# Kernel optimization log

Hardware: AMD Instinct MI355X
Metric: run time of the kernel (lower is better)

The kernel has to match this reference:

```python
import jax, jax.numpy as jnp
import numpy as np

NUM_HEADS = 16
EMB = 1024
HEAD_DIM = EMB // NUM_HEADS


def setup_inputs() -> dict:
    key = jax.random.key(0)
    ks = jax.random.split(key, 9)
    N, L = 2, 2048
    return {
        "keys": jax.random.normal(ks[0], (N, L, EMB), dtype=jnp.float32),
        "queries": jax.random.normal(ks[1], (N, L, EMB), dtype=jnp.float32),
        "values": jax.random.normal(ks[2], (N, L, EMB), dtype=jnp.float32),
        "mask": jax.random.randint(ks[3], (N, L), 0, 2, dtype=jnp.int32),
        "Wk": jax.random.normal(ks[4], (HEAD_DIM, HEAD_DIM), dtype=jnp.float32) * 0.05,
        "Wq": jax.random.normal(ks[5], (HEAD_DIM, HEAD_DIM), dtype=jnp.float32) * 0.05,
        "Wv": jax.random.normal(ks[6], (HEAD_DIM, HEAD_DIM), dtype=jnp.float32) * 0.05,
        "Wo": jax.random.normal(ks[7], (EMB, EMB), dtype=jnp.float32) * 0.02,
        "bo": jax.random.normal(ks[8], (EMB,), dtype=jnp.float32) * 0.02,
    }


def reference(keys, queries, values, mask, Wk, Wq, Wv, Wo, bo):
    N, Q, E = queries.shape
    H, D = NUM_HEADS, HEAD_DIM
    # reshape to heads: [N, L, H, D]
    k = keys.reshape(N, -1, H, D) @ Wk.T
    q = queries.reshape(N, -1, H, D) @ Wq.T
    # faithful to source bug: values are the v-projection of the projected queries
    v = q @ Wv.T
    # energy: [N, H, Q, K]
    energy = jnp.einsum("nqhd,nkhd->nhqk", q, k)
    m = mask[:, None, None, :]  # [N,1,1,K]
    energy = jnp.where(m == 0, jnp.float32(-1e20), energy)
    p = jax.nn.softmax(energy / jnp.sqrt(jnp.float32(E)), axis=3)
    attn = jnp.einsum("nhqk,nkhd->nqhd", p, v).reshape(N, Q, E)
    return attn @ Wo.T + bo
```

## Files before the change

kernel.cpp:

```cpp
#include <hip/hip_runtime.h>
#include <hip/hip_bf16.h>
#include <cmath>

constexpr int N_ = 2;
constexpr int L_ = 2048;
constexpr int H_ = 16;
constexpr int E_ = 1024;
constexpr int ROWS_ = N_ * L_ * H_;
constexpr float KSCALE = 0.04508422002778010648f;

typedef __attribute__((ext_vector_type(8))) short bf16x8;
typedef __attribute__((ext_vector_type(4))) float f32x4;
typedef unsigned short ushort_t;
#define MFMA16(a, b, c) __builtin_amdgcn_mfma_f32_16x16x32_bf16(a, b, c, 0, 0, 0)

__device__ __forceinline__ unsigned short f2bf(float x) {
    union { float f; unsigned u; } v; v.f = x;
    return (unsigned short)((v.u + 0x7fffu + ((v.u >> 16) & 1u)) >> 16);
}
__device__ __forceinline__ unsigned pack2(float a, float b) {
    __hip_bfloat162 t = __float22bfloat162_rn(make_float2(a, b));
    union { __hip_bfloat162 h; unsigned u; } v; v.h = t;
    return v.u;
}
__device__ __forceinline__ void plswap32(unsigned &a, unsigned &b) {
    asm("v_permlane32_swap_b32 %0, %1" : "+v"(a), "+v"(b));
}
__device__ __forceinline__ void plswap16(unsigned &a, unsigned &b) {
    asm("v_permlane16_swap_b32 %0, %1" : "+v"(a), "+v"(b));
}

__global__ __launch_bounds__(256) void proj_kernel(
    const float* __restrict__ keys, const float* __restrict__ queries,
    const float* __restrict__ Wk, const float* __restrict__ Wq, const float* __restrict__ Wv,
    ushort_t* __restrict__ qo, ushort_t* __restrict__ ko, ushort_t* __restrict__ vto)
{
    constexpr int P = 72;
    __shared__ __align__(16) ushort_t Xq[64 * P];
    __shared__ __align__(16) ushort_t Xk[64 * P];
    __shared__ __align__(16) ushort_t Wqs[64 * P];
    __shared__ __align__(16) ushort_t Wks[64 * P];
    __shared__ __align__(16) ushort_t Wvs[64 * P];
    const int tid = threadIdx.x;
    const int lt = blockIdx.x & 31;
    const int h  = (blockIdx.x >> 5) & 15;
    const int n  = blockIdx.x >> 9;
    const int r0 = tid >> 4, c4 = (tid & 15) * 4;

#pragma unroll
    for (int j = 0; j < 4; ++j) {
        const int r = r0 + 16 * j;
        const size_t xoff = (size_t)(n * L_ + lt * 64 + r) * E_ + h * 64 + c4;
        const float4 xq = *(const float4*)&queries[xoff];
        const float4 xk = *(const float4*)&keys[xoff];
        const float4 wq = *(const float4*)&Wq[r * 64 + c4];
        const float4 wk = *(const float4*)&Wk[r * 64 + c4];
        const float4 wv = *(const float4*)&Wv[r * 64 + c4];
        *(uint2*)&Xq[r * P + c4]  = make_uint2(pack2(xq.x, xq.y), pack2(xq.z, xq.w));
        *(uint2*)&Xk[r * P + c4]  = make_uint2(pack2(xk.x, xk.y), pack2(xk.z, xk.w));
        *(uint2*)&Wqs[r * P + c4] = make_uint2(pack2(wq.x, wq.y), pack2(wq.z, wq.w));
        *(uint2*)&Wks[r * P + c4] = make_uint2(pack2(wk.x, wk.y), pack2(wk.z, wk.w));
        *(uint2*)&Wvs[r * P + c4] = make_uint2(pack2(wv.x, wv.y), pack2(wv.z, wv.w));
    }
    __syncthreads();

    const int wave = tid >> 6, lane = tid & 63;
    const int quad = lane >> 4, l16 = lane & 15;
    const int arow = (wave * 16 + l16) * P;
    const f32x4 zero = (f32x4){0.f, 0.f, 0.f, 0.f};

    bf16x8 a0 = *(const bf16x8*)&Xq[arow + quad * 8];
    bf16x8 a1 = *(const bf16x8*)&Xq[arow + 32 + quad * 8];
    bf16x8 c0 = *(const bf16x8*)&Xk[arow + quad * 8];
    bf16x8 c1 = *(const bf16x8*)&Xk[arow + 32 + quad * 8];
    f32x4 qf[4], kf[4];
#pragma unroll
    for (int nt = 0; nt < 4; ++nt) {
        const int brow = (nt * 16 + l16) * P;
        f32x4 acc = MFMA16(a0, *(const bf16x8*)&Wqs[brow + quad * 8], zero);
        qf[nt] = MFMA16(a1, *(const bf16x8*)&Wqs[brow + 32 + quad * 8], acc);
        acc = MFMA16(c0, *(const bf16x8*)&Wks[brow + quad * 8], zero);
        kf[nt] = MFMA16(c1, *(const bf16x8*)&Wks[brow + 32 + quad * 8], acc);
    }
    __syncthreads();

    const int crow = wave * 16 + quad * 4;
#pragma unroll
    for (int nt = 0; nt < 4; ++nt)
#pragma unroll
        for (int reg = 0; reg < 4; ++reg) {
            Xq[(crow + reg) * P + nt * 16 + l16]  = f2bf(qf[nt][reg]);
            Wqs[(crow + reg) * P + nt * 16 + l16] = f2bf(kf[nt][reg] * KSCALE);
        }
    asm volatile("s_waitcnt lgkmcnt(0)" ::: "memory");

    bf16x8 va0 = *(const bf16x8*)&Xq[arow + quad * 8];
    bf16x8 va1 = *(const bf16x8*)&Xq[arow + 32 + quad * 8];
    f32x4 vf[4];
#pragma unroll
    for (int nt = 0; nt < 4; ++nt) {
        const int brow = (nt * 16 + l16) * P;
        f32x4 acc = MFMA16(va0, *(const bf16x8*)&Wvs[brow + quad * 8], zero);
        vf[nt] = MFMA16(va1, *(const bf16x8*)&Wvs[brow + 32 + quad * 8], acc);
    }
#pragma unroll
    for (int nt = 0; nt < 4; ++nt)
#pragma unroll
        for (int reg = 0; reg < 4; ++reg)
            Xk[(nt * 16 + l16) * P + crow + reg] = f2bf(vf[nt][reg]);
    __syncthreads();

#pragma unroll
    for (int j = 0; j < 4; ++j) {
        const int r = r0 + 16 * j;
        const size_t qkoff = (size_t)(n * L_ + lt * 64 + r) * E_ + h * 64 + c4;
        *(uint2*)&qo[qkoff] = *(const uint2*)&Xq[r * P + c4];
        *(uint2*)&ko[qkoff] = *(const uint2*)&Wqs[r * P + c4];
        const size_t vtoff = ((size_t)(n * H_ + h) * 64 + r) * L_ + lt * 64 + c4;
        *(uint2*)&vto[vtoff] = *(const uint2*)&Xk[r * P + c4];
    }
}

__global__ __launch_bounds__(256) void attn_kernel(
    const ushort_t* __restrict__ q, const ushort_t* __restrict__ k,
    const ushort_t* __restrict__ vt, const float* __restrict__ maskf,
    ushort_t* __restrict__ attn)
{
    constexpr int P = 72;
    __shared__ __align__(16) ushort_t Ks[2][64 * P];
    __shared__ __align__(16) ushort_t VTs[2][64 * P];
    __shared__ float Ls[128];

    const int g = blockIdx.x;
    const int xcd = g & 7, j0 = g >> 3;
    const int nh = xcd * 4 + (j0 & 3);
    const int qt = j0 >> 2;
    const int n = nh >> 4, h = nh & 15;

    const int tid = threadIdx.x;
    const int wave = tid >> 6, lane = tid & 63;
    const int l16 = lane & 15, quad = lane >> 4;
    const int r8 = tid >> 3, c8 = (tid & 7) * 8;

    const ushort_t* kh = k  + (size_t)n * L_ * E_ + h * 64;
    const ushort_t* vh = vt + (size_t)(n * H_ + h) * 64 * L_;
    const float*    mh = maskf + n * L_;
    const size_t qrow0 = (size_t)n * L_ + qt * 128 + wave * 32;

    bf16x8 qb[2][2];
#pragma unroll
    for (int s = 0; s < 2; ++s)
#pragma unroll
        for (int c = 0; c < 2; ++c)
            qb[s][c] = *(const bf16x8*)&q[(qrow0 + s * 16 + l16) * E_ + h * 64 + c * 32 + quad * 8];

    uint4 kr[2], vr[2];
#pragma unroll
    for (int j = 0; j < 2; ++j) {
        const int r = r8 + 32 * j;
        kr[j] = *(const uint4*)&kh[(size_t)r * E_ + c8];
        vr[j] = *(const uint4*)&vh[(size_t)r * L_ + c8];
    }
    f32x4 mf[4];
#pragma unroll
    for (int mk = 0; mk < 4; ++mk) mf[mk] = *(const f32x4*)&mh[mk * 16 + quad * 4];

#pragma unroll
    for (int j = 0; j < 2; ++j) {
        const int r = r8 + 32 * j;
        *(uint4*)&Ks[0][r * P + c8]  = kr[j];
        *(uint4*)&VTs[0][r * P + c8] = vr[j];
    }
    __syncthreads();

    float lacc[2] = {0.f, 0.f};
    f32x4 O[2][4];
#pragma unroll
    for (int s = 0; s < 2; ++s)
#pragma unroll
        for (int dt = 0; dt < 4; ++dt) O[s][dt] = (f32x4){0.f, 0.f, 0.f, 0.f};

    for (int t = 0; t < 32; ++t) {
        const int cur = t & 1, nxt = cur ^ 1;
        const int tn = (t < 31) ? t + 1 : 31;

#pragma unroll
        for (int j = 0; j < 2; ++j) {
            const int r = r8 + 32 * j;
            kr[j] = *(const uint4*)&kh[(size_t)(tn * 64 + r) * E_ + c8];
            vr[j] = *(const uint4*)&vh[(size_t)r * L_ + tn * 64 + c8];
        }
        f32x4 mfn[4];
#pragma unroll
        for (int mk = 0; mk < 4; ++mk)
            mfn[mk] = *(const f32x4*)&mh[tn * 64 + mk * 16 + quad * 4];

        bf16x8 kA[4][2];
#pragma unroll
        for (int mk = 0; mk < 4; ++mk)
#pragma unroll
            for (int c = 0; c < 2; ++c)
                kA[mk][c] = *(const bf16x8*)&Ks[cur][(mk * 16 + l16) * P + c * 32 + quad * 8];

        f32x4 sA[2][4];
#pragma unroll
        for (int s = 0; s < 2; ++s)
#pragma unroll
            for (int mk = 0; mk < 4; ++mk) {
                f32x4 acc = mf[mk];
                acc = MFMA16(kA[mk][0], qb[s][0], acc);
                sA[s][mk] = MFMA16(kA[mk][1], qb[s][1], acc);
            }

        bf16x8 vB[4][2];
#pragma unroll
        for (int dt = 0; dt < 4; ++dt)
#pragma unroll
            for (int c = 0; c < 2; ++c)
                vB[dt][c] = *(const bf16x8*)&VTs[cur][(dt * 16 + l16) * P + c * 32 + quad * 8];

        bf16x8 pa[2][2];
#pragma unroll
        for (int s = 0; s < 2; ++s) {
            unsigned u[4][2];
#pragma unroll
            for (int mk = 0; mk < 4; ++mk) {
                const float p0 = __builtin_amdgcn_exp2f(sA[s][mk][0]);
                const float p1 = __builtin_amdgcn_exp2f(sA[s][mk][1]);
                const float p2 = __builtin_amdgcn_exp2f(sA[s][mk][2]);
                const float p3 = __builtin_amdgcn_exp2f(sA[s][mk][3]);
                lacc[s] += (p0 + p1) + (p2 + p3);
                u[mk][0] = pack2(p0, p1);
                u[mk][1] = pack2(p2, p3);
            }
#pragma unroll
            for (int c = 0; c < 2; ++c) {
                union { unsigned w[4]; bf16x8 v; } pw;
#pragma unroll
                for (int hh = 0; hh < 2; ++hh) {
                    unsigned a = u[2 * c][hh], b = u[2 * c + 1][hh];
                    plswap32(a, b);
                    plswap16(a, b);
                    pw.w[hh] = a; pw.w[2 + hh] = b;
                }
                pa[s][c] = pw.v;
            }
        }

#pragma unroll
        for (int s = 0; s < 2; ++s)
#pragma unroll
            for (int dt = 0; dt < 4; ++dt) {
                O[s][dt] = MFMA16(pa[s][0], vB[dt][0], O[s][dt]);
                O[s][dt] = MFMA16(pa[s][1], vB[dt][1], O[s][dt]);
            }

#pragma unroll
        for (int j = 0; j < 2; ++j) {
            const int r = r8 + 32 * j;
            *(uint4*)&Ks[nxt][r * P + c8]  = kr[j];
            *(uint4*)&VTs[nxt][r * P + c8] = vr[j];
        }
#pragma unroll
        for (int mk = 0; mk < 4; ++mk) mf[mk] = mfn[mk];
        __syncthreads();
    }

#pragma unroll
    for (int s = 0; s < 2; ++s) {
        float v = lacc[s];
        v += __shfl_xor(v, 16);
        v += __shfl_xor(v, 32);
        if (quad == 0) Ls[wave * 32 + s * 16 + l16] = 1.f / v;
    }
    asm volatile("s_waitcnt lgkmcnt(0)" ::: "memory");
    f32x4 linv[2];
#pragma unroll
    for (int s = 0; s < 2; ++s) linv[s] = *(const f32x4*)&Ls[wave * 32 + s * 16 + quad * 4];

#pragma unroll
    for (int s = 0; s < 2; ++s)
#pragma unroll
        for (int dt = 0; dt < 4; ++dt)
#pragma unroll
            for (int reg = 0; reg < 4; ++reg) {
                const size_t row = qrow0 + s * 16 + quad * 4 + reg;
                attn[row * E_ + h * 64 + dt * 16 + l16] = f2bf(O[s][dt][reg] * linv[s][reg]);
            }
}

__global__ __launch_bounds__(256) void conv_misc_kernel(
    const float* __restrict__ Wo, const int* __restrict__ mask,
    ushort_t* __restrict__ Wob, float* __restrict__ maskf)
{
    if (blockIdx.x < 1024) {
        const int i = (blockIdx.x * 256 + threadIdx.x) * 4;
        const float4 w = *(const float4*)&Wo[i];
        *(uint2*)&Wob[i] = make_uint2(pack2(w.x, w.y), pack2(w.z, w.w));
    } else {
        const int j = (blockIdx.x - 1024) * 256 + threadIdx.x;
        if (j < N_ * L_) maskf[j] = mask[j] ? 0.f : -1e9f;
    }
}

__global__ __launch_bounds__(256) void outproj_kernel(
    const ushort_t* __restrict__ attn, const ushort_t* __restrict__ Wob,
    const float* __restrict__ bo, float* __restrict__ out)
{
    constexpr int P = 72;
    __shared__ __align__(16) ushort_t As[128 * P];
    __shared__ __align__(16) ushort_t Bs[64 * P];
    const int tid = threadIdx.x;
    const int bc = (blockIdx.x & 15) * 64;
    const int br = (blockIdx.x >> 4) * 128;
    const int r0 = tid >> 4, c4 = (tid & 15) * 4;
    const int wave = tid >> 6, lane = tid & 63;
    const int quad = lane >> 4, l16 = lane & 15;

    uint2 ar[8], brg[4];
#pragma unroll
    for (int j = 0; j < 8; ++j)
        ar[j] = *(const uint2*)&attn[(size_t)(br + r0 + 16 * j) * E_ + c4];
#pragma unroll
    for (int j = 0; j < 4; ++j)
        brg[j] = *(const uint2*)&Wob[(size_t)(bc + r0 + 16 * j) * E_ + c4];

    f32x4 acc[2][4];
#pragma unroll
    for (int s = 0; s < 2; ++s)
#pragma unroll
        for (int nt = 0; nt < 4; ++nt) acc[s][nt] = (f32x4){0.f, 0.f, 0.f, 0.f};

    for (int kt = 0; kt < 16; ++kt) {
#pragma unroll
        for (int j = 0; j < 8; ++j) *(uint2*)&As[(r0 + 16 * j) * P + c4] = ar[j];
#pragma unroll
        for (int j = 0; j < 4; ++j) *(uint2*)&Bs[(r0 + 16 * j) * P + c4] = brg[j];
        __syncthreads();
        const int knext = ((kt < 15) ? (kt + 1) : kt) * 64;
#pragma unroll
        for (int j = 0; j < 8; ++j)
            ar[j] = *(const uint2*)&attn[(size_t)(br + r0 + 16 * j) * E_ + knext + c4];
#pragma unroll
        for (int j = 0; j < 4; ++j)
            brg[j] = *(const uint2*)&Wob[(size_t)(bc + r0 + 16 * j) * E_ + knext + c4];

        bf16x8 aw[2][2], bw[4][2];
#pragma unroll
        for (int s = 0; s < 2; ++s)
#pragma unroll
            for (int c = 0; c < 2; ++c)
                aw[s][c] = *(const bf16x8*)&As[(wave * 32 + s * 16 + l16) * P + c * 32 + quad * 8];
#pragma unroll
        for (int nt = 0; nt < 4; ++nt)
#pragma unroll
            for (int c = 0; c < 2; ++c)
                bw[nt][c] = *(const bf16x8*)&Bs[(nt * 16 + l16) * P + c * 32 + quad * 8];
#pragma unroll
        for (int s = 0; s < 2; ++s)
#pragma unroll
            for (int nt = 0; nt < 4; ++nt) {
                acc[s][nt] = MFMA16(aw[s][0], bw[nt][0], acc[s][nt]);
                acc[s][nt] = MFMA16(aw[s][1], bw[nt][1], acc[s][nt]);
            }
        __syncthreads();
    }
#pragma unroll
    for (int s = 0; s < 2; ++s)
#pragma unroll
        for (int nt = 0; nt < 4; ++nt) {
            const float bias = bo[bc + nt * 16 + l16];
#pragma unroll
            for (int reg = 0; reg < 4; ++reg)
                out[(size_t)(br + wave * 32 + s * 16 + quad * 4 + reg) * E_ + bc + nt * 16 + l16] =
                    acc[s][nt][reg] + bias;
        }
}

extern "C" void kernel_launch(void* const* d_in, const int* in_sizes, int n_in,
                              void* d_out, int out_size, void* d_ws, size_t ws_size,
                              hipStream_t stream)
{
    const float* keys    = (const float*)d_in[0];
    const float* queries = (const float*)d_in[1];
    const int*   mask    = (const int*)d_in[3];
    const float* Wk      = (const float*)d_in[4];
    const float* Wq      = (const float*)d_in[5];
    const float* Wv      = (const float*)d_in[6];
    const float* Wo      = (const float*)d_in[7];
    const float* bo      = (const float*)d_in[8];
    float* out = (float*)d_out;

    ushort_t* qbf  = (ushort_t*)d_ws;
    ushort_t* kbf  = qbf + (size_t)ROWS_ * 64;
    ushort_t* vtbf = kbf + (size_t)ROWS_ * 64;
    ushort_t* abf  = vtbf + (size_t)ROWS_ * 64;
    ushort_t* wob  = abf + (size_t)ROWS_ * 64;
    float*    mskf = (float*)(wob + (size_t)E_ * E_);

    conv_misc_kernel<<<1024 + (N_ * L_ + 255) / 256, 256, 0, stream>>>(Wo, mask, wob, mskf);
    proj_kernel<<<N_ * H_ * (L_ / 64), 256, 0, stream>>>(keys, queries, Wk, Wq, Wv,
                                                         qbf, kbf, vtbf);
    attn_kernel<<<N_ * H_ * (L_ / 128), 256, 0, stream>>>(qbf, kbf, vtbf, mskf, abf);
    outproj_kernel<<<(N_ * L_ / 128) * (E_ / 64), 256, 0, stream>>>(abf, wob, bo, out);
}
```

Measured before the change: 201.4 us.

## Split attention key range across two wave groups with LDS reduction

The attention kernel goes from 256 to 512 threads. Two groups of four waves each process half of every 128-key step, so the loop runs 16 steps instead of 32. At the end, the second group writes its partial O accumulators and row sums to LDS, and the first group adds them, normalises and writes the output. The aim is more waves in flight and more latency hiding per block, at the cost of a larger LDS footprint and an extra reduction plus barrier.

```diff
diff --git a/kernel.cpp b/kernel.cpp
--- a/kernel.cpp
+++ b/kernel.cpp
@@ -121,15 +121,21 @@
     }
 }
 
-__global__ __launch_bounds__(256) void attn_kernel(
+__global__ __launch_bounds__(512, 4) void attn_kernel(
     const ushort_t* __restrict__ q, const ushort_t* __restrict__ k,
     const ushort_t* __restrict__ vt, const float* __restrict__ maskf,
     ushort_t* __restrict__ attn)
 {
-    constexpr int P = 72;
-    __shared__ __align__(16) ushort_t Ks[2][64 * P];
-    __shared__ __align__(16) ushort_t VTs[2][64 * P];
-    __shared__ float Ls[128];
+    constexpr int PK = 72;
+    constexpr int PV = 136;
+    constexpr int KP_SZ = 128 * PK;
+    constexpr int VP_SZ = 64 * PV;
+    __shared__ __align__(16) unsigned char SMEM[(2 * KP_SZ + 2 * VP_SZ) * 2 + 512];
+    ushort_t* Kp = (ushort_t*)SMEM;
+    ushort_t* Vp = (ushort_t*)(SMEM + 2 * KP_SZ * 2);
+    float*    Ls = (float*)(SMEM + (2 * KP_SZ + 2 * VP_SZ) * 2);
+    float*    Oc = (float*)SMEM;
+    float*    Lp = (float*)(SMEM + 2 * KP_SZ * 2);
 
     const int g = blockIdx.x;
     const int xcd = g & 7, j0 = g >> 3;
@@ -140,76 +146,75 @@
     const int tid = threadIdx.x;
     const int wave = tid >> 6, lane = tid & 63;
     const int l16 = lane & 15, quad = lane >> 4;
+    const int qg = wave & 3, kg = wave >> 2;
     const int r8 = tid >> 3, c8 = (tid & 7) * 8;
+    const int vr8 = tid >> 4, vc8 = (tid & 15) * 8;
 
     const ushort_t* kh = k  + (size_t)n * L_ * E_ + h * 64;
     const ushort_t* vh = vt + (size_t)(n * H_ + h) * 64 * L_;
     const float*    mh = maskf + n * L_;
-    const size_t qrow0 = (size_t)n * L_ + qt * 128 + wave * 32;
+    const size_t qrow0 = (size_t)n * L_ + qt * 128 + qg * 32;
 
     bf16x8 qb[2][2];
 #pragma unroll
-    for (int s = 0; s < 2; ++s)
+    for (int st = 0; st < 2; ++st)
 #pragma unroll
         for (int c = 0; c < 2; ++c)
-            qb[s][c] = *(const bf16x8*)&q[(qrow0 + s * 16 + l16) * E_ + h * 64 + c * 32 + quad * 8];
+            qb[st][c] = *(const bf16x8*)&q[(qrow0 + st * 16 + l16) * E_ + h * 64 + c * 32 + quad * 8];
 
     uint4 kr[2], vr[2];
 #pragma unroll
     for (int j = 0; j < 2; ++j) {
-        const int r = r8 + 32 * j;
-        kr[j] = *(const uint4*)&kh[(size_t)r * E_ + c8];
-        vr[j] = *(const uint4*)&vh[(size_t)r * L_ + c8];
+        kr[j] = *(const uint4*)&kh[(size_t)(64 * j + r8) * E_ + c8];
+        vr[j] = *(const uint4*)&vh[(size_t)(vr8 + 32 * j) * L_ + vc8];
     }
     f32x4 mf[4];
 #pragma unroll
-    for (int mk = 0; mk < 4; ++mk) mf[mk] = *(const f32x4*)&mh[mk * 16 + quad * 4];
+    for (int mk = 0; mk < 4; ++mk) mf[mk] = *(const f32x4*)&mh[kg * 64 + mk * 16 + quad * 4];
 
 #pragma unroll
     for (int j = 0; j < 2; ++j) {
-        const int r = r8 + 32 * j;
-        *(uint4*)&Ks[0][r * P + c8]  = kr[j];
-        *(uint4*)&VTs[0][r * P + c8] = vr[j];
+        *(uint4*)&Kp[(64 * j + r8) * PK + c8]  = kr[j];
+        *(uint4*)&Vp[(vr8 + 32 * j) * PV + vc8] = vr[j];
     }
     __syncthreads();
 
     float lacc[2] = {0.f, 0.f};
     f32x4 O[2][4];
 #pragma unroll
-    for (int s = 0; s < 2; ++s)
-#pragma unroll
-        for (int dt = 0; dt < 4; ++dt) O[s][dt] = (f32x4){0.f, 0.f, 0.f, 0.f};
-
-    for (int t = 0; t < 32; ++t) {
-        const int cur = t & 1, nxt = cur ^ 1;
-        const int tn = (t < 31) ? t + 1 : 31;
+    for (int st = 0; st < 2; ++st)
+#pragma unroll
+        for (int dt = 0; dt < 4; ++dt) O[st][dt] = (f32x4){0.f, 0.f, 0.f, 0.f};
+
+    for (int s = 0; s < 16; ++s) {
+        const int cur = s & 1, nxt = cur ^ 1;
+        const int sn = (s < 15) ? s + 1 : 15;
 
 #pragma unroll
         for (int j = 0; j < 2; ++j) {
-            const int r = r8 + 32 * j;
-            kr[j] = *(const uint4*)&kh[(size_t)(tn * 64 + r) * E_ + c8];
-            vr[j] = *(const uint4*)&vh[(size_t)r * L_ + tn * 64 + c8];
+            kr[j] = *(const uint4*)&kh[(size_t)(128 * sn + 64 * j + r8) * E_ + c8];
+            vr[j] = *(const uint4*)&vh[(size_t)(vr8 + 32 * j) * L_ + 128 * sn + vc8];
         }
         f32x4 mfn[4];
 #pragma unroll
         for (int mk = 0; mk < 4; ++mk)
-            mfn[mk] = *(const f32x4*)&mh[tn * 64 + mk * 16 + quad * 4];
+            mfn[mk] = *(const f32x4*)&mh[128 * sn + kg * 64 + mk * 16 + quad * 4];
 
         bf16x8 kA[4][2];
 #pragma unroll
         for (int mk = 0; mk < 4; ++mk)
 #pragma unroll
             for (int c = 0; c < 2; ++c)
-                kA[mk][c] = *(const bf16x8*)&Ks[cur][(mk * 16 + l16) * P + c * 32 + quad * 8];
+                kA[mk][c] = *(const bf16x8*)&Kp[cur * KP_SZ + (kg * 64 + mk * 16 + l16) * PK + c * 32 + quad * 8];
 
         f32x4 sA[2][4];
 #pragma unroll
-        for (int s = 0; s < 2; ++s)
+        for (int st = 0; st < 2; ++st)
 #pragma unroll
             for (int mk = 0; mk < 4; ++mk) {
                 f32x4 acc = mf[mk];
-                acc = MFMA16(kA[mk][0], qb[s][0], acc);
-                sA[s][mk] = MFMA16(kA[mk][1], qb[s][1], acc);
+                acc = MFMA16(kA[mk][0], qb[st][0], acc);
+                sA[st][mk] = MFMA16(kA[mk][1], qb[st][1], acc);
             }
 
         bf16x8 vB[4][2];
@@ -217,19 +222,19 @@
         for (int dt = 0; dt < 4; ++dt)
 #pragma unroll
             for (int c = 0; c < 2; ++c)
-                vB[dt][c] = *(const bf16x8*)&VTs[cur][(dt * 16 + l16) * P + c * 32 + quad * 8];
+                vB[dt][c] = *(const bf16x8*)&Vp[cur * VP_SZ + (dt * 16 + l16) * PV + kg * 64 + c * 32 + quad * 8];
 
         bf16x8 pa[2][2];
 #pragma unroll
-        for (int s = 0; s < 2; ++s) {
+        for (int st = 0; st < 2; ++st) {
             unsigned u[4][2];
 #pragma unroll
             for (int mk = 0; mk < 4; ++mk) {
-                const float p0 = __builtin_amdgcn_exp2f(sA[s][mk][0]);
-                const float p1 = __builtin_amdgcn_exp2f(sA[s][mk][1]);
-                const float p2 = __builtin_amdgcn_exp2f(sA[s][mk][2]);
-                const float p3 = __builtin_amdgcn_exp2f(sA[s][mk][3]);
-                lacc[s] += (p0 + p1) + (p2 + p3);
+                const float p0 = __builtin_amdgcn_exp2f(sA[st][mk][0]);
+                const float p1 = __builtin_amdgcn_exp2f(sA[st][mk][1]);
+                const float p2 = __builtin_amdgcn_exp2f(sA[st][mk][2]);
+                const float p3 = __builtin_amdgcn_exp2f(sA[st][mk][3]);
+                lacc[st] += (p0 + p1) + (p2 + p3);
                 u[mk][0] = pack2(p0, p1);
                 u[mk][1] = pack2(p2, p3);
             }
@@ -243,50 +248,75 @@
                     plswap16(a, b);
                     pw.w[hh] = a; pw.w[2 + hh] = b;
                 }
-                pa[s][c] = pw.v;
-            }
-        }
-
-#pragma unroll
-        for (int s = 0; s < 2; ++s)
+                pa[st][c] = pw.v;
+            }
+        }
+
+#pragma unroll
+        for (int st = 0; st < 2; ++st)
 #pragma unroll
             for (int dt = 0; dt < 4; ++dt) {
-                O[s][dt] = MFMA16(pa[s][0], vB[dt][0], O[s][dt]);
-                O[s][dt] = MFMA16(pa[s][1], vB[dt][1], O[s][dt]);
+                O[st][dt] = MFMA16(pa[st][0], vB[dt][0], O[st][dt]);
+                O[st][dt] = MFMA16(pa[st][1], vB[dt][1], O[st][dt]);
             }
 
 #pragma unroll
         for (int j = 0; j < 2; ++j) {
-            const int r = r8 + 32 * j;
-            *(uint4*)&Ks[nxt][r * P + c8]  = kr[j];
-            *(uint4*)&VTs[nxt][r * P + c8] = vr[j];
+            *(uint4*)&Kp[nxt * KP_SZ + (64 * j + r8) * PK + c8]   = kr[j];
+            *(uint4*)&Vp[nxt * VP_SZ + (vr8 + 32 * j) * PV + vc8] = vr[j];
         }
 #pragma unroll
         for (int mk = 0; mk < 4; ++mk) mf[mk] = mfn[mk];
         __syncthreads();
     }
 
-#pragma unroll
-    for (int s = 0; s < 2; ++s) {
-        float v = lacc[s];
+    float vsum[2];
+#pragma unroll
+    for (int st = 0; st < 2; ++st) {
+        float v = lacc[st];
         v += __shfl_xor(v, 16);
         v += __shfl_xor(v, 32);
-        if (quad == 0) Ls[wave * 32 + s * 16 + l16] = 1.f / v;
-    }
-    asm volatile("s_waitcnt lgkmcnt(0)" ::: "memory");
-    f32x4 linv[2];
-#pragma unroll
-    for (int s = 0; s < 2; ++s) linv[s] = *(const f32x4*)&Ls[wave * 32 + s * 16 + quad * 4];
-
-#pragma unroll
-    for (int s = 0; s < 2; ++s)
-#pragma unroll
-        for (int dt = 0; dt < 4; ++dt)
-#pragma unroll
-            for (int reg = 0; reg < 4; ++reg) {
-                const size_t row = qrow0 + s * 16 + quad * 4 + reg;
-                attn[row * E_ + h * 64 + dt * 16 + l16] = f2bf(O[s][dt][reg] * linv[s][reg]);
-            }
+        vsum[st] = v;
+    }
+
+    if (kg == 1) {
+#pragma unroll
+        for (int st = 0; st < 2; ++st) {
+            if (quad == 0) Lp[qg * 32 + st * 16 + l16] = vsum[st];
+#pragma unroll
+            for (int dt = 0; dt < 4; ++dt)
+                *(f32x4*)&Oc[(dt * 16 + l16) * 132 + qg * 32 + st * 16 + quad * 4] = O[st][dt];
+        }
+    }
+    __syncthreads();
+
+    if (kg == 0) {
+#pragma unroll
+        for (int st = 0; st < 2; ++st) {
+#pragma unroll
+            for (int dt = 0; dt < 4; ++dt) {
+                const f32x4 op = *(const f32x4*)&Oc[(dt * 16 + l16) * 132 + qg * 32 + st * 16 + quad * 4];
+                O[st][dt] += op;
+            }
+            const float vtot = vsum[st] + Lp[qg * 32 + st * 16 + l16];
+            if (quad == 0) Ls[qg * 32 + st * 16 + l16] = 1.f / vtot;
+        }
+        asm volatile("s_waitcnt lgkmcnt(0)" ::: "memory");
+        f32x4 linv[2];
+#pragma unroll
+        for (int st = 0; st < 2; ++st)
+            linv[st] = *(const f32x4*)&Ls[qg * 32 + st * 16 + quad * 4];
+
+#pragma unroll
+        for (int st = 0; st < 2; ++st)
+#pragma unroll
+            for (int dt = 0; dt < 4; ++dt)
+#pragma unroll
+                for (int reg = 0; reg < 4; ++reg) {
+                    const size_t row = qrow0 + st * 16 + quad * 4 + reg;
+                    attn[row * E_ + h * 64 + dt * 16 + l16] = f2bf(O[st][dt][reg] * linv[st][reg]);
+                }
+    }
 }
 
 __global__ __launch_bounds__(256) void conv_misc_kernel(
@@ -401,6 +431,6 @@
     conv_misc_kernel<<<1024 + (N_ * L_ + 255) / 256, 256, 0, stream>>>(Wo, mask, wob, mskf);
     proj_kernel<<<N_ * H_ * (L_ / 64), 256, 0, stream>>>(keys, queries, Wk, Wq, Wv,
                                                          qbf, kbf, vtbf);
-    attn_kernel<<<N_ * H_ * (L_ / 128), 256, 0, stream>>>(qbf, kbf, vtbf, mskf, abf);
+    attn_kernel<<<N_ * H_ * (L_ / 128), 512, 0, stream>>>(qbf, kbf, vtbf, mskf, abf);
     outproj_kernel<<<(N_ * L_ / 128) * (E_ / 64), 256, 0, stream>>>(abf, wob, bo, out);
 }
```

Measured after the change: 183.4 us. 8.9% less time.
